# Kernel optimization log

Hardware: AMD Instinct MI355X
Metric: run time of the kernel (lower is better)

The kernel has to match this reference:

```python
import jax, jax.numpy as jnp
import numpy as np

N = 50000      # nodes
E = 800000     # edges (avg degree 16)
F_IN = 128     # node_feat_dim
D = 128        # d_model
E_DIM = 64     # edge_dim
H = 4          # heads


def setup_inputs() -> dict:
    key = jax.random.key(0)
    ks = jax.random.split(key, 32)
    inp = {
        "x": jax.random.normal(ks[0], (N, F_IN), jnp.float32),
        "edge_index": jax.random.randint(ks[1], (2, E), 0, N, dtype=jnp.int64),
        "edge_attr": jax.random.normal(ks[2], (E, E_DIM), jnp.float32),
        "lp_W": jax.random.normal(ks[3], (F_IN, D), jnp.float32) * 0.05,
        "lp_b": jnp.zeros((D,), jnp.float32),
    }
    i = 4
    for l in (1, 2, 3):
        inp[f"W{l}"] = jax.random.normal(ks[i], (D, D), jnp.float32) * 0.05; i += 1
        inp[f"as{l}"] = jax.random.normal(ks[i], (H, D // H), jnp.float32) * 0.05; i += 1
        inp[f"ad{l}"] = jax.random.normal(ks[i], (H, D // H), jnp.float32) * 0.05; i += 1
        inp[f"We{l}"] = jax.random.normal(ks[i], (E_DIM, D), jnp.float32) * 0.05; i += 1
        inp[f"ae{l}"] = jax.random.normal(ks[i], (H, D // H), jnp.float32) * 0.05; i += 1
        inp[f"b{l}"] = jnp.zeros((D,), jnp.float32); i += 1
    return inp


def _segment_softmax(logits, seg, n):
    m = jax.ops.segment_max(logits, seg, num_segments=n)       # [N,H]
    ex = jnp.exp(logits - m[seg])
    s = jax.ops.segment_sum(ex, seg, num_segments=n)
    return ex / s[seg]


def _gat_conv(x, src, dst, e, W, a_s, a_d, We, a_e, b):
    # PyG GATConv(d, d//H, H, edge_dim=E_DIM, aggr='mean'), concat=True
    n = x.shape[0]
    C = W.shape[1] // H
    xh = (x @ W).reshape(n, H, C)            # shared lin for src/dst
    eh = (e @ We).reshape(-1, H, C)
    logit = (xh * a_s).sum(-1)[src] + (xh * a_d).sum(-1)[dst] + (eh * a_e).sum(-1)  # [Etot,H]
    att = _segment_softmax(jax.nn.leaky_relu(logit, 0.2), dst, n)
    agg = jax.ops.segment_sum(xh[src] * att[:, :, None], dst, num_segments=n)       # [N,H,C]
    cnt = jnp.maximum(jax.ops.segment_sum(jnp.ones((src.shape[0],), x.dtype), dst, num_segments=n), 1.0)
    out = agg / cnt[:, None, None]           # aggr='mean'
    return out.reshape(n, H * C) + b


def reference(x, edge_index, edge_attr, lp_W, lp_b,
              W1, as1, ad1, We1, ae1, b1,
              W2, as2, ad2, We2, ae2, b2,
              W3, as3, ad3, We3, ae3, b3):
    n = x.shape[0]
    src, dst = edge_index[0], edge_index[1]
    # add_self_loops with fill_value='mean': self-loop attr = mean of incoming edge attrs
    deg = jnp.maximum(jax.ops.segment_sum(jnp.ones((src.shape[0],), x.dtype), dst, num_segments=n), 1.0)
    loop_attr = jax.ops.segment_sum(edge_attr, dst, num_segments=n) / deg[:, None]
    ar = jnp.arange(n, dtype=src.dtype)
    src_sl = jnp.concatenate([src, ar])
    dst_sl = jnp.concatenate([dst, ar])
    e_sl = jnp.concatenate([edge_attr, loop_attr], axis=0)

    h = x @ lp_W + lp_b
    h = jax.nn.relu(h + _gat_conv(h, src_sl, dst_sl, e_sl, W1, as1, ad1, We1, ae1, b1))
    h = jax.nn.relu(h + _gat_conv(h, src_sl, dst_sl, e_sl, W2, as2, ad2, We2, ae2, b2))
    h = jax.nn.relu(h + _gat_conv(h, src_sl, dst_sl, e_sl, W3, as3, ad3, We3, ae3, b3))
    return h
```

## Files before the change

### kernel.cpp

```cpp
#include <hip/hip_runtime.h>
#include <cmath>

#define HEADS 4
#define DM 128
#define EDIM 64

__device__ __forceinline__ float wred_max(float v) {
    #pragma unroll
    for (int off = 32; off; off >>= 1) v = fmaxf(v, __shfl_xor(v, off, 64));
    return v;
}
__device__ __forceinline__ float wred_sum(float v) {
    #pragma unroll
    for (int off = 32; off; off >>= 1) v += __shfl_xor(v, off, 64);
    return v;
}

__global__ void k_deg(const int* __restrict__ dst, int* __restrict__ deg, int E) {
    int e = blockIdx.x * blockDim.x + threadIdx.x;
    if (e < E) atomicAdd(&deg[dst[e]], 1);
}

__global__ void k_scan1(const int* __restrict__ deg, int* __restrict__ partial,
                        int* __restrict__ bsums, int N) {
    __shared__ int s[256];
    int n = blockIdx.x * 256 + threadIdx.x;
    int v = (n < N) ? (deg[n] + 1) : 0;
    s[threadIdx.x] = v;
    __syncthreads();
    for (int off = 1; off < 256; off <<= 1) {
        int t = (threadIdx.x >= off) ? s[threadIdx.x - off] : 0;
        __syncthreads();
        s[threadIdx.x] += t;
        __syncthreads();
    }
    if (n < N) partial[n] = s[threadIdx.x];
    if (threadIdx.x == 255) bsums[blockIdx.x] = s[255];
}
__global__ void k_scan2(int* __restrict__ bsums, int nb) {
    __shared__ int s[256];
    int v = (threadIdx.x < nb) ? bsums[threadIdx.x] : 0;
    s[threadIdx.x] = v;
    __syncthreads();
    for (int off = 1; off < 256; off <<= 1) {
        int t = (threadIdx.x >= off) ? s[threadIdx.x - off] : 0;
        __syncthreads();
        s[threadIdx.x] += t;
        __syncthreads();
    }
    bsums[threadIdx.x] = s[threadIdx.x];
}
__global__ void k_scan3(const int* __restrict__ partial, const int* __restrict__ bsums,
                        int* __restrict__ row_ptr, int N) {
    int n = blockIdx.x * 256 + threadIdx.x;
    if (n >= N) return;
    int add = (blockIdx.x > 0) ? bsums[blockIdx.x - 1] : 0;
    row_ptr[n + 1] = partial[n] + add;
    if (n == 0) row_ptr[0] = 0;
}

__global__ void k_csr_fill(const int* __restrict__ ei, int* __restrict__ cursor,
                           int* __restrict__ eid, int* __restrict__ src_csr,
                           int* __restrict__ epos, int E, int Etot) {
    int e = blockIdx.x * blockDim.x + threadIdx.x;
    if (e >= Etot) return;
    int s, d;
    if (e < E) { s = ei[e]; d = ei[E + e]; }
    else { s = e - E; d = e - E; }
    int pos = atomicAdd(&cursor[d], 1);
    eid[pos] = e;
    src_csr[pos] = s;
    epos[e] = pos;
}

__global__ void k_loop_gather(const int* __restrict__ row_ptr, const int* __restrict__ eid,
                              const float* __restrict__ ea, float* __restrict__ loop_attr,
                              int N, int E) {
    int w = blockIdx.x * 4 + (threadIdx.x >> 6);
    int lane = threadIdx.x & 63;
    if (w >= N) return;
    int beg = row_ptr[w], end = row_ptr[w + 1];
    float acc = 0.f;
    for (int i = beg; i < end; ++i) {
        int e = eid[i];
        if (e < E) acc += ea[(size_t)e * EDIM + lane];
    }
    float d = fmaxf((float)(end - beg - 1), 1.0f);
    loop_attr[(size_t)w * EDIM + lane] = acc / d;
}

__global__ void k_prep_v(const float* __restrict__ We1, const float* __restrict__ ae1,
                         const float* __restrict__ We2, const float* __restrict__ ae2,
                         const float* __restrict__ We3, const float* __restrict__ ae3,
                         float* __restrict__ vg) {
    int j = threadIdx.x;
    const float* Wes[3] = {We1, We2, We3};
    const float* aes[3] = {ae1, ae2, ae3};
    for (; j < EDIM * 12; j += 256) {
        int k = j / 12, m = j % 12;
        int l = m >> 2, h = m & 3;
        const float* We = Wes[l];
        const float* ae = aes[l];
        float acc = 0.f;
        #pragma unroll
        for (int c = 0; c < 32; ++c) acc += We[k * DM + h * 32 + c] * ae[h * 32 + c];
        vg[j] = acc;
    }
}

__global__ __launch_bounds__(256) void k_alpha_e2(const float* __restrict__ ea,
                                                  const float* __restrict__ loop_attr,
                                                  const float* __restrict__ vg,
                                                  float* __restrict__ alpha_e,
                                                  int E, int Etot) {
    __shared__ float vT[12][64];
    for (int j = threadIdx.x; j < EDIM * 12; j += 256) {
        int k = j & 63, m = j >> 6;
        vT[m][k] = vg[k * 12 + m];
    }
    __syncthreads();
    int base = (blockIdx.x * 256 + threadIdx.x) * 4;
    const float4* rows[4];
    #pragma unroll
    for (int i = 0; i < 4; ++i) {
        int e = base + i;
        if (e < Etot)
            rows[i] = (e < E) ? (const float4*)(ea + (size_t)e * EDIM)
                              : (const float4*)(loop_attr + (size_t)(e - E) * EDIM);
        else
            rows[i] = (const float4*)ea;
    }
    float acc[4][12];
    #pragma unroll
    for (int i = 0; i < 4; ++i)
        #pragma unroll
        for (int m = 0; m < 12; ++m) acc[i][m] = 0.f;
    #pragma unroll 4
    for (int k4 = 0; k4 < 16; ++k4) {
        float4 evv[4];
        #pragma unroll
        for (int i = 0; i < 4; ++i) evv[i] = rows[i][k4];
        #pragma unroll
        for (int m = 0; m < 12; ++m) {
            float4 vv = *(const float4*)&vT[m][k4 * 4];
            #pragma unroll
            for (int i = 0; i < 4; ++i) {
                acc[i][m] += evv[i].x * vv.x + evv[i].y * vv.y +
                             evv[i].z * vv.z + evv[i].w * vv.w;
            }
        }
    }
    #pragma unroll
    for (int i = 0; i < 4; ++i) {
        int e = base + i;
        if (e >= Etot) continue;
        #pragma unroll
        for (int l = 0; l < 3; ++l) {
            float4 o = make_float4(acc[i][l * 4 + 0], acc[i][l * 4 + 1],
                                   acc[i][l * 4 + 2], acc[i][l * 4 + 3]);
            *(float4*)&alpha_e[((size_t)l * Etot + e) * HEADS] = o;
        }
    }
}

__global__ __launch_bounds__(256) void k_gemm128v2(const float* __restrict__ A,
                                                   const float* __restrict__ W,
                                                   const float* __restrict__ bias,
                                                   float* __restrict__ out, int M) {
    __shared__ float Wl[DM * DM];
    int tx = threadIdx.x;
    {
        float4* Wl4 = (float4*)Wl;
        const float4* W4 = (const float4*)W;
        for (int i = tx; i < DM * DM / 4; i += 256) Wl4[i] = W4[i];
    }
    __syncthreads();
    int colg = tx & 31;
    int row0 = blockIdx.x * 32 + (tx >> 5) * 4;
    const float* aptr[4];
    bool valid[4];
    #pragma unroll
    for (int r = 0; r < 4; ++r) {
        int rr = row0 + r;
        valid[r] = rr < M;
        aptr[r] = A + (size_t)(valid[r] ? rr : (M - 1)) * DM;
    }
    float4 acc[4] = {{0,0,0,0},{0,0,0,0},{0,0,0,0},{0,0,0,0}};
    for (int k4 = 0; k4 < DM / 4; ++k4) {
        float4 a4[4];
        #pragma unroll
        for (int r = 0; r < 4; ++r) a4[r] = *(const float4*)&aptr[r][k4 * 4];
        #pragma unroll
        for (int j = 0; j < 4; ++j) {
            float4 w4 = *(const float4*)&Wl[(k4 * 4 + j) * DM + colg * 4];
            #pragma unroll
            for (int r = 0; r < 4; ++r) {
                float av = ((const float*)&a4[r])[j];
                acc[r].x += av * w4.x;
                acc[r].y += av * w4.y;
                acc[r].z += av * w4.z;
                acc[r].w += av * w4.w;
            }
        }
    }
    float4 bv = {0, 0, 0, 0};
    if (bias) bv = *(const float4*)&bias[colg * 4];
    #pragma unroll
    for (int r = 0; r < 4; ++r) {
        if (!valid[r]) continue;
        float4 o = make_float4(acc[r].x + bv.x, acc[r].y + bv.y,
                               acc[r].z + bv.z, acc[r].w + bv.w);
        *(float4*)&out[(size_t)(row0 + r) * DM + colg * 4] = o;
    }
}

__global__ void k_attn_coeff(const float* __restrict__ xh, const float* __restrict__ a_s,
                             const float* __restrict__ a_d, float* __restrict__ as_n,
                             float* __restrict__ ad_n, int N) {
    int i = blockIdx.x * blockDim.x + threadIdx.x;
    if (i >= N * HEADS) return;
    int n = i >> 2, h = i & 3;
    const float* v = xh + (size_t)n * DM + h * 32;
    float s1 = 0.f, s2 = 0.f;
    #pragma unroll
    for (int c = 0; c < 32; ++c) {
        float xv = v[c];
        s1 += xv * a_s[h * 32 + c];
        s2 += xv * a_d[h * 32 + c];
    }
    as_n[i] = s1;
    ad_n[i] = s2;
}

__global__ void k_logits(const int* __restrict__ ei, const int* __restrict__ epos,
                         const float* __restrict__ as_n, const float* __restrict__ ad_n,
                         const float* __restrict__ alpha_e_l, float* __restrict__ att_s,
                         int E, int Etot) {
    int e = blockIdx.x * blockDim.x + threadIdx.x;
    if (e >= Etot) return;
    int s, d;
    if (e < E) { s = ei[e]; d = ei[E + e]; }
    else { s = e - E; d = e - E; }
    float4 as4 = *(const float4*)&as_n[s * HEADS];
    float4 ad4 = *(const float4*)&ad_n[d * HEADS];
    float4 al4 = *(const float4*)&alpha_e_l[(size_t)e * HEADS];
    float4 o;
    float l0 = as4.x + ad4.x + al4.x; o.x = (l0 >= 0.f) ? l0 : 0.2f * l0;
    float l1 = as4.y + ad4.y + al4.y; o.y = (l1 >= 0.f) ? l1 : 0.2f * l1;
    float l2 = as4.z + ad4.z + al4.z; o.z = (l2 >= 0.f) ? l2 : 0.2f * l2;
    float l3 = as4.w + ad4.w + al4.w; o.w = (l3 >= 0.f) ? l3 : 0.2f * l3;
    *(float4*)&att_s[(size_t)epos[e] * HEADS] = o;
}

__global__ void k_softmax(const int* __restrict__ row_ptr, float* __restrict__ att_s, int N) {
    int w = blockIdx.x * 4 + (threadIdx.x >> 6);
    int lane = threadIdx.x & 63;
    if (w >= N) return;
    int beg = row_ptr[w], end = row_ptr[w + 1];
    const float4* a4 = (const float4*)att_s;
    float m0 = -INFINITY, m1 = -INFINITY, m2 = -INFINITY, m3 = -INFINITY;
    for (int i = beg + lane; i < end; i += 64) {
        float4 a = a4[i];
        m0 = fmaxf(m0, a.x); m1 = fmaxf(m1, a.y);
        m2 = fmaxf(m2, a.z); m3 = fmaxf(m3, a.w);
    }
    m0 = wred_max(m0); m1 = wred_max(m1); m2 = wred_max(m2); m3 = wred_max(m3);
    float s0 = 0.f, s1 = 0.f, s2 = 0.f, s3 = 0.f;
    for (int i = beg + lane; i < end; i += 64) {
        float4 a = a4[i];
        s0 += __expf(a.x - m0); s1 += __expf(a.y - m1);
        s2 += __expf(a.z - m2); s3 += __expf(a.w - m3);
    }
    s0 = wred_sum(s0); s1 = wred_sum(s1); s2 = wred_sum(s2); s3 = wred_sum(s3);
    float r0 = 1.f / s0, r1 = 1.f / s1, r2 = 1.f / s2, r3 = 1.f / s3;
    for (int i = beg + lane; i < end; i += 64) {
        float4 a = a4[i];
        float4 o = make_float4(__expf(a.x - m0) * r0, __expf(a.y - m1) * r1,
                               __expf(a.z - m2) * r2, __expf(a.w - m3) * r3);
        *(float4*)&att_s[(size_t)i * HEADS] = o;
    }
}

__global__ void k_aggregate(const int* __restrict__ row_ptr, const int* __restrict__ src_csr,
                            const float* __restrict__ att_s, const float* __restrict__ xh,
                            const float* __restrict__ hin, const float* __restrict__ bias,
                            float* __restrict__ hout, int N) {
    int w = blockIdx.x * 4 + (threadIdx.x >> 6);
    int lane = threadIdx.x & 63;
    if (w >= N) return;
    int beg = row_ptr[w], end = row_ptr[w + 1];
    int f0 = lane, f1 = lane + 64;
    int h0 = lane >> 5;
    int h1 = 2 + (lane >> 5);
    float acc0 = 0.f, acc1 = 0.f;
    for (int i = beg; i < end; ++i) {
        int s = src_csr[i];
        float a0 = att_s[(size_t)i * HEADS + h0];
        float a1 = att_s[(size_t)i * HEADS + h1];
        acc0 += a0 * xh[(size_t)s * DM + f0];
        acc1 += a1 * xh[(size_t)s * DM + f1];
    }
    float cnt = (float)(end - beg);
    float o0 = acc0 / cnt + bias[f0] + hin[(size_t)w * DM + f0];
    float o1 = acc1 / cnt + bias[f1] + hin[(size_t)w * DM + f1];
    hout[(size_t)w * DM + f0] = fmaxf(o0, 0.f);
    hout[(size_t)w * DM + f1] = fmaxf(o1, 0.f);
}

extern "C" void kernel_launch(void* const* d_in, const int* in_sizes, int n_in,
                              void* d_out, int out_size, void* d_ws, size_t ws_size,
                              hipStream_t stream) {
    const float* x = (const float*)d_in[0];
    const int* ei = (const int*)d_in[1];
    const float* edge_attr = (const float*)d_in[2];
    const float* lp_W = (const float*)d_in[3];
    const float* lp_b = (const float*)d_in[4];
    int N = in_sizes[0] / DM;
    int E = in_sizes[1] / 2;
    int Etot = E + N;
    float* out = (float*)d_out;

    char* p = (char*)d_ws;
    auto alloc = [&](size_t bytes) {
        char* r = p;
        p += (bytes + 255) & ~(size_t)255;
        return r;
    };
    float* h = (float*)alloc((size_t)N * DM * 4);
    float* xh = (float*)alloc((size_t)N * DM * 4);
    float* loop_attr = (float*)alloc((size_t)N * EDIM * 4);
    float* alpha_e = (float*)alloc((size_t)3 * Etot * HEADS * 4);
    float* att_s = (float*)alloc((size_t)Etot * HEADS * 4);
    float* as_n = (float*)alloc((size_t)N * HEADS * 4);
    float* ad_n = (float*)alloc((size_t)N * HEADS * 4);
    float* vg = (float*)alloc(EDIM * 12 * 4);
    int* deg = (int*)alloc((size_t)N * 4);
    int* row_ptr = (int*)alloc((size_t)(N + 1) * 4);
    int* partial = (int*)alloc((size_t)N * 4);
    int* eid = (int*)alloc((size_t)Etot * 4);
    int* src_csr = (int*)alloc((size_t)Etot * 4);
    int* epos = (int*)alloc((size_t)Etot * 4);
    int* bsums = (int*)alloc(256 * 4);
    int* cursor = partial;

    hipMemsetAsync(deg, 0, (size_t)N * 4, stream);

    k_deg<<<(E + 255) / 256, 256, 0, stream>>>(ei + E, deg, E);

    int nb = (N + 255) / 256;
    k_scan1<<<nb, 256, 0, stream>>>(deg, partial, bsums, N);
    k_scan2<<<1, 256, 0, stream>>>(bsums, nb);
    k_scan3<<<nb, 256, 0, stream>>>(partial, bsums, row_ptr, N);
    hipMemcpyAsync(cursor, row_ptr, (size_t)N * 4, hipMemcpyDeviceToDevice, stream);
    k_csr_fill<<<(Etot + 255) / 256, 256, 0, stream>>>(ei, cursor, eid, src_csr, epos, E, Etot);
    k_loop_gather<<<(N + 3) / 4, 256, 0, stream>>>(row_ptr, eid, edge_attr, loop_attr, N, E);

    k_prep_v<<<1, 256, 0, stream>>>((const float*)d_in[8], (const float*)d_in[9],
                                    (const float*)d_in[14], (const float*)d_in[15],
                                    (const float*)d_in[20], (const float*)d_in[21], vg);
    k_alpha_e2<<<(Etot + 1023) / 1024, 256, 0, stream>>>(edge_attr, loop_attr, vg,
                                                         alpha_e, E, Etot);

    k_gemm128v2<<<(N + 31) / 32, 256, 0, stream>>>(x, lp_W, lp_b, h, N);

    for (int l = 0; l < 3; ++l) {
        const float* W = (const float*)d_in[5 + 6 * l];
        const float* a_s = (const float*)d_in[6 + 6 * l];
        const float* a_d = (const float*)d_in[7 + 6 * l];
        const float* b = (const float*)d_in[10 + 6 * l];
        k_gemm128v2<<<(N + 31) / 32, 256, 0, stream>>>(h, W, nullptr, xh, N);
        k_attn_coeff<<<(N * HEADS + 255) / 256, 256, 0, stream>>>(xh, a_s, a_d, as_n, ad_n, N);
        k_logits<<<(Etot + 255) / 256, 256, 0, stream>>>(ei, epos, as_n, ad_n,
                                                         alpha_e + (size_t)l * Etot * HEADS,
                                                         att_s, E, Etot);
        k_softmax<<<(N + 3) / 4, 256, 0, stream>>>(row_ptr, att_s, N);
        float* hout = (l == 2) ? out : h;
        k_aggregate<<<(N + 3) / 4, 256, 0, stream>>>(row_ptr, src_csr, att_s, xh, h, b, hout, N);
    }
}
```

Baseline: 1.285 ms.

## Fuse logits, softmax and aggregation; store edge alphas in CSR order

Merges the per-layer logits, segment softmax and aggregation kernels into one wave-per-node kernel. It computes logits from CSR-ordered source indices and keeps exp values in LDS when the degree is at most 128, with a recompute fallback for larger degrees. Edge attention terms are written directly in CSR order. Self-loop terms are computed by averaging the neighbours' alpha values (linearity) instead of gathering full edge-attribute rows, which removes the loop_attr pass and the eid array. This cuts global traffic for the att_s buffer and saves several launches, at the cost of more LDS use per block and an in-place kernel inside the aggregation (`hin` and `hout` point to the same buffer).

```diff
diff --git a/kernel.cpp b/kernel.cpp
--- a/kernel.cpp
+++ b/kernel.cpp
@@ -4,6 +4,7 @@
 #define HEADS 4
 #define DM 128
 #define EDIM 64
+#define CAP 128
 
 __device__ __forceinline__ float wred_max(float v) {
     #pragma unroll
@@ -60,33 +61,16 @@
 }
 
 __global__ void k_csr_fill(const int* __restrict__ ei, int* __restrict__ cursor,
-                           int* __restrict__ eid, int* __restrict__ src_csr,
-                           int* __restrict__ epos, int E, int Etot) {
+                           int* __restrict__ src_csr, int* __restrict__ epos,
+                           int E, int Etot) {
     int e = blockIdx.x * blockDim.x + threadIdx.x;
     if (e >= Etot) return;
     int s, d;
     if (e < E) { s = ei[e]; d = ei[E + e]; }
     else { s = e - E; d = e - E; }
     int pos = atomicAdd(&cursor[d], 1);
-    eid[pos] = e;
     src_csr[pos] = s;
     epos[e] = pos;
-}
-
-__global__ void k_loop_gather(const int* __restrict__ row_ptr, const int* __restrict__ eid,
-                              const float* __restrict__ ea, float* __restrict__ loop_attr,
-                              int N, int E) {
-    int w = blockIdx.x * 4 + (threadIdx.x >> 6);
-    int lane = threadIdx.x & 63;
-    if (w >= N) return;
-    int beg = row_ptr[w], end = row_ptr[w + 1];
-    float acc = 0.f;
-    for (int i = beg; i < end; ++i) {
-        int e = eid[i];
-        if (e < E) acc += ea[(size_t)e * EDIM + lane];
-    }
-    float d = fmaxf((float)(end - beg - 1), 1.0f);
-    loop_attr[(size_t)w * EDIM + lane] = acc / d;
 }
 
 __global__ void k_prep_v(const float* __restrict__ We1, const float* __restrict__ ae1,
@@ -108,10 +92,10 @@
     }
 }
 
-__global__ __launch_bounds__(256) void k_alpha_e2(const float* __restrict__ ea,
-                                                  const float* __restrict__ loop_attr,
+__global__ __launch_bounds__(256) void k_alpha_e3(const float* __restrict__ ea,
+                                                  const int* __restrict__ epos,
                                                   const float* __restrict__ vg,
-                                                  float* __restrict__ alpha_e,
+                                                  float* __restrict__ alpha_s,
                                                   int E, int Etot) {
     __shared__ float vT[12][64];
     for (int j = threadIdx.x; j < EDIM * 12; j += 256) {
@@ -120,16 +104,7 @@
     }
     __syncthreads();
     int base = (blockIdx.x * 256 + threadIdx.x) * 4;
-    const float4* rows[4];
-    #pragma unroll
-    for (int i = 0; i < 4; ++i) {
-        int e = base + i;
-        if (e < Etot)
-            rows[i] = (e < E) ? (const float4*)(ea + (size_t)e * EDIM)
-                              : (const float4*)(loop_attr + (size_t)(e - E) * EDIM);
-        else
-            rows[i] = (const float4*)ea;
-    }
+    if (base >= E) return;
     float acc[4][12];
     #pragma unroll
     for (int i = 0; i < 4; ++i)
@@ -139,7 +114,11 @@
     for (int k4 = 0; k4 < 16; ++k4) {
         float4 evv[4];
         #pragma unroll
-        for (int i = 0; i < 4; ++i) evv[i] = rows[i][k4];
+        for (int i = 0; i < 4; ++i) {
+            int e = base + i;
+            evv[i] = (e < E) ? *(const float4*)(ea + (size_t)e * EDIM + k4 * 4)
+                             : make_float4(0.f, 0.f, 0.f, 0.f);
+        }
         #pragma unroll
         for (int m = 0; m < 12; ++m) {
             float4 vv = *(const float4*)&vT[m][k4 * 4];
@@ -153,14 +132,40 @@
     #pragma unroll
     for (int i = 0; i < 4; ++i) {
         int e = base + i;
-        if (e >= Etot) continue;
+        if (e >= E) continue;
+        int pos = epos[e];
         #pragma unroll
         for (int l = 0; l < 3; ++l) {
             float4 o = make_float4(acc[i][l * 4 + 0], acc[i][l * 4 + 1],
                                    acc[i][l * 4 + 2], acc[i][l * 4 + 3]);
-            *(float4*)&alpha_e[((size_t)l * Etot + e) * HEADS] = o;
-        }
-    }
+            *(float4*)&alpha_s[((size_t)l * Etot + pos) * HEADS] = o;
+        }
+    }
+}
+
+__global__ void k_self_alpha(const int* __restrict__ row_ptr, const int* __restrict__ epos,
+                             float* __restrict__ alpha_s, int N, int E, int Etot) {
+    int n = blockIdx.x * 256 + threadIdx.x;
+    if (n >= N) return;
+    int beg = row_ptr[n], end = row_ptr[n + 1];
+    int self = epos[E + n];
+    float4 s0 = {0, 0, 0, 0}, s1 = {0, 0, 0, 0}, s2 = {0, 0, 0, 0};
+    float* a0 = alpha_s;
+    float* a1 = alpha_s + (size_t)Etot * HEADS;
+    float* a2 = alpha_s + (size_t)2 * Etot * HEADS;
+    for (int i = beg; i < end; ++i) {
+        if (i == self) continue;
+        float4 v0 = *(const float4*)&a0[(size_t)i * HEADS];
+        float4 v1 = *(const float4*)&a1[(size_t)i * HEADS];
+        float4 v2 = *(const float4*)&a2[(size_t)i * HEADS];
+        s0.x += v0.x; s0.y += v0.y; s0.z += v0.z; s0.w += v0.w;
+        s1.x += v1.x; s1.y += v1.y; s1.z += v1.z; s1.w += v1.w;
+        s2.x += v2.x; s2.y += v2.y; s2.z += v2.z; s2.w += v2.w;
+    }
+    float r = 1.f / fmaxf((float)(end - beg - 1), 1.0f);
+    *(float4*)&a0[(size_t)self * HEADS] = make_float4(s0.x * r, s0.y * r, s0.z * r, s0.w * r);
+    *(float4*)&a1[(size_t)self * HEADS] = make_float4(s1.x * r, s1.y * r, s1.z * r, s1.w * r);
+    *(float4*)&a2[(size_t)self * HEADS] = make_float4(s2.x * r, s2.y * r, s2.z * r, s2.w * r);
 }
 
 __global__ __launch_bounds__(256) void k_gemm128v2(const float* __restrict__ A,
@@ -232,79 +237,119 @@
     ad_n[i] = s2;
 }
 
-__global__ void k_logits(const int* __restrict__ ei, const int* __restrict__ epos,
-                         const float* __restrict__ as_n, const float* __restrict__ ad_n,
-                         const float* __restrict__ alpha_e_l, float* __restrict__ att_s,
-                         int E, int Etot) {
-    int e = blockIdx.x * blockDim.x + threadIdx.x;
-    if (e >= Etot) return;
-    int s, d;
-    if (e < E) { s = ei[e]; d = ei[E + e]; }
-    else { s = e - E; d = e - E; }
-    float4 as4 = *(const float4*)&as_n[s * HEADS];
-    float4 ad4 = *(const float4*)&ad_n[d * HEADS];
-    float4 al4 = *(const float4*)&alpha_e_l[(size_t)e * HEADS];
-    float4 o;
-    float l0 = as4.x + ad4.x + al4.x; o.x = (l0 >= 0.f) ? l0 : 0.2f * l0;
-    float l1 = as4.y + ad4.y + al4.y; o.y = (l1 >= 0.f) ? l1 : 0.2f * l1;
-    float l2 = as4.z + ad4.z + al4.z; o.z = (l2 >= 0.f) ? l2 : 0.2f * l2;
-    float l3 = as4.w + ad4.w + al4.w; o.w = (l3 >= 0.f) ? l3 : 0.2f * l3;
-    *(float4*)&att_s[(size_t)epos[e] * HEADS] = o;
-}
-
-__global__ void k_softmax(const int* __restrict__ row_ptr, float* __restrict__ att_s, int N) {
-    int w = blockIdx.x * 4 + (threadIdx.x >> 6);
+__global__ __launch_bounds__(256) void k_attn_fused(
+        const int* __restrict__ row_ptr, const int* __restrict__ src_csr,
+        const float* __restrict__ alpha_l, const float* __restrict__ as_n,
+        const float* __restrict__ ad_n, const float* __restrict__ xh,
+        const float* __restrict__ hin, const float* __restrict__ bias,
+        float* __restrict__ hout, int N) {
+    __shared__ float sm[4][CAP][HEADS];
+    int wv = threadIdx.x >> 6;
     int lane = threadIdx.x & 63;
+    int w = blockIdx.x * 4 + wv;
     if (w >= N) return;
     int beg = row_ptr[w], end = row_ptr[w + 1];
-    const float4* a4 = (const float4*)att_s;
+    int cnt = end - beg;
+    float4 ad4 = *(const float4*)&ad_n[w * HEADS];
     float m0 = -INFINITY, m1 = -INFINITY, m2 = -INFINITY, m3 = -INFINITY;
-    for (int i = beg + lane; i < end; i += 64) {
-        float4 a = a4[i];
-        m0 = fmaxf(m0, a.x); m1 = fmaxf(m1, a.y);
-        m2 = fmaxf(m2, a.z); m3 = fmaxf(m3, a.w);
-    }
-    m0 = wred_max(m0); m1 = wred_max(m1); m2 = wred_max(m2); m3 = wred_max(m3);
     float s0 = 0.f, s1 = 0.f, s2 = 0.f, s3 = 0.f;
-    for (int i = beg + lane; i < end; i += 64) {
-        float4 a = a4[i];
-        s0 += __expf(a.x - m0); s1 += __expf(a.y - m1);
-        s2 += __expf(a.z - m2); s3 += __expf(a.w - m3);
-    }
-    s0 = wred_sum(s0); s1 = wred_sum(s1); s2 = wred_sum(s2); s3 = wred_sum(s3);
-    float r0 = 1.f / s0, r1 = 1.f / s1, r2 = 1.f / s2, r3 = 1.f / s3;
-    for (int i = beg + lane; i < end; i += 64) {
-        float4 a = a4[i];
-        float4 o = make_float4(__expf(a.x - m0) * r0, __expf(a.y - m1) * r1,
-                               __expf(a.z - m2) * r2, __expf(a.w - m3) * r3);
-        *(float4*)&att_s[(size_t)i * HEADS] = o;
-    }
-}
-
-__global__ void k_aggregate(const int* __restrict__ row_ptr, const int* __restrict__ src_csr,
-                            const float* __restrict__ att_s, const float* __restrict__ xh,
-                            const float* __restrict__ hin, const float* __restrict__ bias,
-                            float* __restrict__ hout, int N) {
-    int w = blockIdx.x * 4 + (threadIdx.x >> 6);
-    int lane = threadIdx.x & 63;
-    if (w >= N) return;
-    int beg = row_ptr[w], end = row_ptr[w + 1];
-    int f0 = lane, f1 = lane + 64;
-    int h0 = lane >> 5;
-    int h1 = 2 + (lane >> 5);
-    float acc0 = 0.f, acc1 = 0.f;
-    for (int i = beg; i < end; ++i) {
-        int s = src_csr[i];
-        float a0 = att_s[(size_t)i * HEADS + h0];
-        float a1 = att_s[(size_t)i * HEADS + h1];
-        acc0 += a0 * xh[(size_t)s * DM + f0];
-        acc1 += a1 * xh[(size_t)s * DM + f1];
-    }
-    float cnt = (float)(end - beg);
-    float o0 = acc0 / cnt + bias[f0] + hin[(size_t)w * DM + f0];
-    float o1 = acc1 / cnt + bias[f1] + hin[(size_t)w * DM + f1];
-    hout[(size_t)w * DM + f0] = fmaxf(o0, 0.f);
-    hout[(size_t)w * DM + f1] = fmaxf(o1, 0.f);
+    if (cnt <= CAP) {
+        for (int i = beg + lane; i < end; i += 64) {
+            int s = src_csr[i];
+            float4 as4 = *(const float4*)&as_n[s * HEADS];
+            float4 al4 = *(const float4*)&alpha_l[(size_t)i * HEADS];
+            float l0 = as4.x + ad4.x + al4.x; l0 = (l0 >= 0.f) ? l0 : 0.2f * l0;
+            float l1 = as4.y + ad4.y + al4.y; l1 = (l1 >= 0.f) ? l1 : 0.2f * l1;
+            float l2 = as4.z + ad4.z + al4.z; l2 = (l2 >= 0.f) ? l2 : 0.2f * l2;
+            float l3 = as4.w + ad4.w + al4.w; l3 = (l3 >= 0.f) ? l3 : 0.2f * l3;
+            *(float4*)&sm[wv][i - beg][0] = make_float4(l0, l1, l2, l3);
+            m0 = fmaxf(m0, l0); m1 = fmaxf(m1, l1);
+            m2 = fmaxf(m2, l2); m3 = fmaxf(m3, l3);
+        }
+        m0 = wred_max(m0); m1 = wred_max(m1); m2 = wred_max(m2); m3 = wred_max(m3);
+        for (int i = beg + lane; i < end; i += 64) {
+            float4 l4 = *(const float4*)&sm[wv][i - beg][0];
+            float e0 = __expf(l4.x - m0), e1 = __expf(l4.y - m1);
+            float e2 = __expf(l4.z - m2), e3 = __expf(l4.w - m3);
+            *(float4*)&sm[wv][i - beg][0] = make_float4(e0, e1, e2, e3);
+            s0 += e0; s1 += e1; s2 += e2; s3 += e3;
+        }
+        s0 = wred_sum(s0); s1 = wred_sum(s1); s2 = wred_sum(s2); s3 = wred_sum(s3);
+        int h0 = lane >> 5;
+        float rA = (h0 ? 1.f / s1 : 1.f / s0);
+        float rB = (h0 ? 1.f / s3 : 1.f / s2);
+        int f0 = lane, f1 = lane + 64;
+        float acc0 = 0.f, acc1 = 0.f;
+        int j = 0;
+        for (; j + 1 < cnt; j += 2) {
+            int sA = src_csr[beg + j];
+            int sB = src_csr[beg + j + 1];
+            float aA0 = sm[wv][j][h0], aA1 = sm[wv][j][2 + h0];
+            float aB0 = sm[wv][j + 1][h0], aB1 = sm[wv][j + 1][2 + h0];
+            float xA0 = xh[(size_t)sA * DM + f0], xA1 = xh[(size_t)sA * DM + f1];
+            float xB0 = xh[(size_t)sB * DM + f0], xB1 = xh[(size_t)sB * DM + f1];
+            acc0 += aA0 * xA0 + aB0 * xB0;
+            acc1 += aA1 * xA1 + aB1 * xB1;
+        }
+        if (j < cnt) {
+            int sA = src_csr[beg + j];
+            acc0 += sm[wv][j][h0] * xh[(size_t)sA * DM + f0];
+            acc1 += sm[wv][j][2 + h0] * xh[(size_t)sA * DM + f1];
+        }
+        float rc = 1.f / (float)cnt;
+        float o0 = acc0 * rA * rc + bias[f0] + hin[(size_t)w * DM + f0];
+        float o1 = acc1 * rB * rc + bias[f1] + hin[(size_t)w * DM + f1];
+        hout[(size_t)w * DM + f0] = fmaxf(o0, 0.f);
+        hout[(size_t)w * DM + f1] = fmaxf(o1, 0.f);
+    } else {
+        for (int i = beg + lane; i < end; i += 64) {
+            int s = src_csr[i];
+            float4 as4 = *(const float4*)&as_n[s * HEADS];
+            float4 al4 = *(const float4*)&alpha_l[(size_t)i * HEADS];
+            float l0 = as4.x + ad4.x + al4.x; l0 = (l0 >= 0.f) ? l0 : 0.2f * l0;
+            float l1 = as4.y + ad4.y + al4.y; l1 = (l1 >= 0.f) ? l1 : 0.2f * l1;
+            float l2 = as4.z + ad4.z + al4.z; l2 = (l2 >= 0.f) ? l2 : 0.2f * l2;
+            float l3 = as4.w + ad4.w + al4.w; l3 = (l3 >= 0.f) ? l3 : 0.2f * l3;
+            m0 = fmaxf(m0, l0); m1 = fmaxf(m1, l1);
+            m2 = fmaxf(m2, l2); m3 = fmaxf(m3, l3);
+        }
+        m0 = wred_max(m0); m1 = wred_max(m1); m2 = wred_max(m2); m3 = wred_max(m3);
+        for (int i = beg + lane; i < end; i += 64) {
+            int s = src_csr[i];
+            float4 as4 = *(const float4*)&as_n[s * HEADS];
+            float4 al4 = *(const float4*)&alpha_l[(size_t)i * HEADS];
+            float l0 = as4.x + ad4.x + al4.x; l0 = (l0 >= 0.f) ? l0 : 0.2f * l0;
+            float l1 = as4.y + ad4.y + al4.y; l1 = (l1 >= 0.f) ? l1 : 0.2f * l1;
+            float l2 = as4.z + ad4.z + al4.z; l2 = (l2 >= 0.f) ? l2 : 0.2f * l2;
+            float l3 = as4.w + ad4.w + al4.w; l3 = (l3 >= 0.f) ? l3 : 0.2f * l3;
+            s0 += __expf(l0 - m0); s1 += __expf(l1 - m1);
+            s2 += __expf(l2 - m2); s3 += __expf(l3 - m3);
+        }
+        s0 = wred_sum(s0); s1 = wred_sum(s1); s2 = wred_sum(s2); s3 = wred_sum(s3);
+        int h0 = lane >> 5;
+        float rA = (h0 ? 1.f / s1 : 1.f / s0);
+        float rB = (h0 ? 1.f / s3 : 1.f / s2);
+        float mA = (h0 ? m1 : m0), mB = (h0 ? m3 : m2);
+        int f0 = lane, f1 = lane + 64;
+        float acc0 = 0.f, acc1 = 0.f;
+        for (int j = 0; j < cnt; ++j) {
+            int i = beg + j;
+            int s = src_csr[i];
+            float asA = as_n[s * HEADS + h0], asB = as_n[s * HEADS + 2 + h0];
+            float adA = (h0 ? ad4.y : ad4.x), adB = (h0 ? ad4.w : ad4.z);
+            float alA = alpha_l[(size_t)i * HEADS + h0];
+            float alB = alpha_l[(size_t)i * HEADS + 2 + h0];
+            float lA = asA + adA + alA; lA = (lA >= 0.f) ? lA : 0.2f * lA;
+            float lB = asB + adB + alB; lB = (lB >= 0.f) ? lB : 0.2f * lB;
+            acc0 += __expf(lA - mA) * xh[(size_t)s * DM + f0];
+            acc1 += __expf(lB - mB) * xh[(size_t)s * DM + f1];
+        }
+        float rc = 1.f / (float)cnt;
+        float o0 = acc0 * rA * rc + bias[f0] + hin[(size_t)w * DM + f0];
+        float o1 = acc1 * rB * rc + bias[f1] + hin[(size_t)w * DM + f1];
+        hout[(size_t)w * DM + f0] = fmaxf(o0, 0.f);
+        hout[(size_t)w * DM + f1] = fmaxf(o1, 0.f);
+    }
 }
 
 extern "C" void kernel_launch(void* const* d_in, const int* in_sizes, int n_in,
@@ -328,16 +373,13 @@
     };
     float* h = (float*)alloc((size_t)N * DM * 4);
     float* xh = (float*)alloc((size_t)N * DM * 4);
-    float* loop_attr = (float*)alloc((size_t)N * EDIM * 4);
-    float* alpha_e = (float*)alloc((size_t)3 * Etot * HEADS * 4);
-    float* att_s = (float*)alloc((size_t)Etot * HEADS * 4);
+    float* alpha_s = (float*)alloc((size_t)3 * Etot * HEADS * 4);
     float* as_n = (float*)alloc((size_t)N * HEADS * 4);
     float* ad_n = (float*)alloc((size_t)N * HEADS * 4);
     float* vg = (float*)alloc(EDIM * 12 * 4);
     int* deg = (int*)alloc((size_t)N * 4);
     int* row_ptr = (int*)alloc((size_t)(N + 1) * 4);
     int* partial = (int*)alloc((size_t)N * 4);
-    int* eid = (int*)alloc((size_t)Etot * 4);
     int* src_csr = (int*)alloc((size_t)Etot * 4);
     int* epos = (int*)alloc((size_t)Etot * 4);
     int* bsums = (int*)alloc(256 * 4);
@@ -352,14 +394,13 @@
     k_scan2<<<1, 256, 0, stream>>>(bsums, nb);
     k_scan3<<<nb, 256, 0, stream>>>(partial, bsums, row_ptr, N);
     hipMemcpyAsync(cursor, row_ptr, (size_t)N * 4, hipMemcpyDeviceToDevice, stream);
-    k_csr_fill<<<(Etot + 255) / 256, 256, 0, stream>>>(ei, cursor, eid, src_csr, epos, E, Etot);
-    k_loop_gather<<<(N + 3) / 4, 256, 0, stream>>>(row_ptr, eid, edge_attr, loop_attr, N, E);
+    k_csr_fill<<<(Etot + 255) / 256, 256, 0, stream>>>(ei, cursor, src_csr, epos, E, Etot);
 
     k_prep_v<<<1, 256, 0, stream>>>((const float*)d_in[8], (const float*)d_in[9],
                                     (const float*)d_in[14], (const float*)d_in[15],
                                     (const float*)d_in[20], (const float*)d_in[21], vg);
-    k_alpha_e2<<<(Etot + 1023) / 1024, 256, 0, stream>>>(edge_attr, loop_attr, vg,
-                                                         alpha_e, E, Etot);
+    k_alpha_e3<<<(E + 1023) / 1024, 256, 0, stream>>>(edge_attr, epos, vg, alpha_s, E, Etot);
+    k_self_alpha<<<(N + 255) / 256, 256, 0, stream>>>(row_ptr, epos, alpha_s, N, E, Etot);
 
     k_gemm128v2<<<(N + 31) / 32, 256, 0, stream>>>(x, lp_W, lp_b, h, N);
 
@@ -370,11 +411,9 @@
         const float* b = (const float*)d_in[10 + 6 * l];
         k_gemm128v2<<<(N + 31) / 32, 256, 0, stream>>>(h, W, nullptr, xh, N);
         k_attn_coeff<<<(N * HEADS + 255) / 256, 256, 0, stream>>>(xh, a_s, a_d, as_n, ad_n, N);
-        k_logits<<<(Etot + 255) / 256, 256, 0, stream>>>(ei, epos, as_n, ad_n,
-                                                         alpha_e + (size_t)l * Etot * HEADS,
-                                                         att_s, E, Etot);
-        k_softmax<<<(N + 3) / 4, 256, 0, stream>>>(row_ptr, att_s, N);
         float* hout = (l == 2) ? out : h;
-        k_aggregate<<<(N + 3) / 4, 256, 0, stream>>>(row_ptr, src_csr, att_s, xh, h, b, hout, N);
-    }
-}
+        k_attn_fused<<<(N + 3) / 4, 256, 0, stream>>>(row_ptr, src_csr,
+                                                      alpha_s + (size_t)l * Etot * HEADS,
+                                                      as_n, ad_n, xh, h, b, hout, N);
+    }
+}
```

After: 1.029 ms. -19.9%, faster.
